# Kernel optimization log

Measured on AMD Instinct MI355X. Metric: run time of the kernel, lower is better.

## Reference

```python
import jax, jax.numpy as jnp
import numpy as np
import math

N_FRAG = 500_000
N_GENES = 5000
N_FREQ = 20
ENC_DIM = N_FREQ * 2 * 2  # 80
EMB_DIM = 5


def setup_inputs() -> dict:
    key = jax.random.key(0)
    k1, k2, k3, k4 = jax.random.split(key, 4)
    coordinates = jax.random.normal(k1, (N_FRAG, 2), dtype=jnp.float32) * 1000.0
    gene_ix = jax.random.randint(k2, (N_FRAG,), 0, N_GENES, dtype=jnp.int64 if jax.config.jax_enable_x64 else jnp.int32)
    # disjoint contiguous groups covering all fragments: 100k groups of 2, 50k of 3, 25k of 4, 10k of 5
    n2 = jnp.arange(0, 200_000, dtype=jnp.int32)
    n3 = jnp.arange(200_000, 350_000, dtype=jnp.int32)
    n4 = jnp.arange(350_000, 450_000, dtype=jnp.int32)
    n5 = jnp.arange(450_000, 500_000, dtype=jnp.int32)
    stdv = 1.0 / math.sqrt(EMB_DIM)
    weight1 = jax.random.uniform(k3, (N_GENES, ENC_DIM, EMB_DIM), dtype=jnp.float32, minval=-stdv, maxval=stdv)
    weight2 = jax.random.uniform(k4, (N_GENES, ENC_DIM, EMB_DIM), dtype=jnp.float32, minval=-stdv, maxval=stdv)
    return {"coordinates": coordinates, "gene_ix": gene_ix, "n2": n2, "n3": n3, "n4": n4, "n5": n5,
            "weight1": weight1, "weight2": weight2}


def _sine_encoding(coordinates):
    # frequencies: each of the N_FREQ frequencies repeated twice; shifts alternate (0, pi/2)
    i = jnp.arange(1, N_FREQ + 1, dtype=coordinates.dtype)
    freqs = jnp.repeat(1.0 / 1000.0 ** (2.0 * i / N_FREQ), 2)            # [2*N_FREQ]
    shifts = jnp.tile(jnp.array([0.0, jnp.pi / 2], coordinates.dtype), N_FREQ)  # [2*N_FREQ]
    # [N, 2, 1] * [2*N_FREQ] -> [N, 2, 2*N_FREQ] -> flatten -> [N, ENC_DIM]
    return jnp.sin(coordinates[..., None] * freqs + shifts).reshape(coordinates.shape[0], -1)


def _group_self_attention(emb, enc_dim_unused, groups):
    # groups: list of (group_size, flat index array); disjoint sets of fragment rows
    D = emb.shape[-1]
    for i, n_ in groups:
        x = emb[n_].reshape(-1, i, D)                                    # [G, i, D]
        scores = jnp.einsum('gid,gjd->gij', x, x) / math.sqrt(i)         # scale by sqrt(group size)
        y = jnp.einsum('gij,gjd->gid', jax.nn.softmax(scores, axis=-1), x)
        emb = emb.at[n_].set(y.reshape(-1, D))
    return emb


def reference(coordinates, gene_ix, n2, n3, n4, n5, weight1, weight2):
    enc = _sine_encoding(coordinates)                                    # [N, 80]
    # per-fragment gather of gene weight matrix, contract over encoding dim
    emb = jax.nn.sigmoid(jnp.einsum('ne,ned->nd', enc, weight1[gene_ix]))  # [N, 5]
    # NOTE: original forward computes embedding_att from weight2 but never uses it (dead code)
    emb = _group_self_attention(emb, enc, [(2, n2), (3, n3), (4, n4), (5, n5)])
    return emb
```

## Files before the change

### kernel.cpp

```cpp
#include <hip/hip_runtime.h>
#include <hip/hip_bf16.h>
#include <math.h>

#define N_FRAG 500000
#define N_GENES 5000
#define EMB_DIM 5
#define NFREQ 20
#define NR 8
#define SECCAP 64
#define GCAP (NR * SECCAP)
#define CURSTRIDE 16
#define CURN 5120
#define SCAT_BLOCKS ((N_FRAG + 255) / 256)
#define CHUNKS_PER_GENE 3
#define NTASKS (N_GENES * CHUNKS_PER_GENE)
#define EMB_BLOCKS ((NTASKS + 3) / 4)
#define ATTN_BLOCKS 723

static constexpr float FREQS[20] = {
    5.011872336272722e-01f, 2.511886431509580e-01f, 1.258925411794167e-01f,
    6.309573444801933e-02f, 3.162277660168379e-02f, 1.584893192461113e-02f,
    7.943282347242814e-03f, 3.981071705534973e-03f, 1.995262314968880e-03f,
    1.000000000000000e-03f, 5.011872336272725e-04f, 2.511886431509580e-04f,
    1.258925411794167e-04f, 6.309573444801934e-05f, 3.162277660168379e-05f,
    1.584893192461114e-05f, 7.943282347242822e-06f, 3.981071705534973e-06f,
    1.995262314968879e-06f, 1.000000000000000e-06f
};
#define INV2PI 0.15915494309189535f

__global__ void __launch_bounds__(256) scatter_xcd_kernel(
    const int* __restrict__ gene_ix,
    int* __restrict__ cursor, int* __restrict__ sortedN)
{
    int xcd;
    asm volatile("s_getreg_b32 %0, hwreg(HW_REG_XCC_ID)" : "=s"(xcd));
    const int r = xcd & (NR - 1);

    int i = blockIdx.x * blockDim.x + threadIdx.x;
    if (i >= N_FRAG) return;
    int g = gene_ix[i];
    int pos = atomicAdd(&cursor[((size_t)r * CURN + g) * CURSTRIDE], 1);
    if (pos < SECCAP)
        sortedN[(size_t)g * GCAP + r * SECCAP + pos] = i;
}

__global__ void __launch_bounds__(256) emb_wave_kernel(
    const int* __restrict__ cursor, const int* __restrict__ sortedN,
    const float* __restrict__ coords, const float* __restrict__ w1,
    float* __restrict__ out)
{
    __shared__ float wlds[4][400];
    const int wv   = threadIdx.x >> 6;
    const int lane = threadIdx.x & 63;
    const int task = blockIdx.x * 4 + wv;
    if (task >= NTASKS) return;
    const int g     = task / CHUNKS_PER_GENE;
    const int chunk = task - CHUNKS_PER_GENE * g;

    int c0 = min(cursor[((size_t)0 * CURN + g) * CURSTRIDE], SECCAP);
    int c1 = min(cursor[((size_t)1 * CURN + g) * CURSTRIDE], SECCAP);
    int c2 = min(cursor[((size_t)2 * CURN + g) * CURSTRIDE], SECCAP);
    int c3 = min(cursor[((size_t)3 * CURN + g) * CURSTRIDE], SECCAP);
    int c4 = min(cursor[((size_t)4 * CURN + g) * CURSTRIDE], SECCAP);
    int c5 = min(cursor[((size_t)5 * CURN + g) * CURSTRIDE], SECCAP);
    int c6 = min(cursor[((size_t)6 * CURN + g) * CURSTRIDE], SECCAP);
    int c7 = min(cursor[((size_t)7 * CURN + g) * CURSTRIDE], SECCAP);
    int S1 = c0, S2 = S1 + c1, S3 = S2 + c2, S4 = S3 + c3;
    int S5 = S4 + c4, S6 = S5 + c5, S7 = S6 + c6;
    int total = S7 + c7;

    if (chunk * 64 >= total) return;

    const float4* __restrict__ Wg4 =
        reinterpret_cast<const float4*>(w1 + (size_t)g * 400);
    float4* wl4 = reinterpret_cast<float4*>(&wlds[wv][0]);
    if (lane < 50) {
        float4 wa = Wg4[lane];
        float4 wb = Wg4[lane + 50];
        wl4[lane]      = wa;
        wl4[lane + 50] = wb;
    }

    const int cid = chunk * 64 + lane;
    const bool active = cid < total;

    int r = (cid >= S1) + (cid >= S2) + (cid >= S3) + (cid >= S4)
          + (cid >= S5) + (cid >= S6) + (cid >= S7);
    int Sr = 0;
    Sr = (r == 1) ? S1 : Sr;  Sr = (r == 2) ? S2 : Sr;
    Sr = (r == 3) ? S3 : Sr;  Sr = (r == 4) ? S4 : Sr;
    Sr = (r == 5) ? S5 : Sr;  Sr = (r == 6) ? S6 : Sr;
    Sr = (r == 7) ? S7 : Sr;
    int idx = cid - Sr;

    float cx = 0.f, cy = 0.f; int n = 0;
    if (active) {
        n = sortedN[(size_t)g * GCAP + r * SECCAP + idx];
        float2 c = reinterpret_cast<const float2*>(coords)[n];
        cx = c.x; cy = c.y;
    }

    const float* __restrict__ W = &wlds[wv][0];
    float a0 = 0.f, a1 = 0.f, a2 = 0.f, a3 = 0.f, a4 = 0.f;
#pragma unroll
    for (int k = 0; k < NFREQ; ++k) {
        const float gf = FREQS[k] * INV2PI;
        float rx = cx * gf; rx -= floorf(rx);
        float ry = cy * gf; ry -= floorf(ry);
        float s0 = __builtin_amdgcn_sinf(rx);
        float c0f = __builtin_amdgcn_cosf(rx);
        float s1 = __builtin_amdgcn_sinf(ry);
        float c1f = __builtin_amdgcn_cosf(ry);

        const float* p0 = W + 10 * k;
        const float* p1 = W + 200 + 10 * k;
        a0 = fmaf(s0, p0[0], fmaf(c0f, p0[5], fmaf(s1, p1[0], fmaf(c1f, p1[5], a0))));
        a1 = fmaf(s0, p0[1], fmaf(c0f, p0[6], fmaf(s1, p1[1], fmaf(c1f, p1[6], a1))));
        a2 = fmaf(s0, p0[2], fmaf(c0f, p0[7], fmaf(s1, p1[2], fmaf(c1f, p1[7], a2))));
        a3 = fmaf(s0, p0[3], fmaf(c0f, p0[8], fmaf(s1, p1[3], fmaf(c1f, p1[8], a3))));
        a4 = fmaf(s0, p0[4], fmaf(c0f, p0[9], fmaf(s1, p1[4], fmaf(c1f, p1[9], a4))));
    }

    if (active) {
        float* o = out + (size_t)n * EMB_DIM;
        o[0] = 1.f / (1.f + __expf(-a0));
        o[1] = 1.f / (1.f + __expf(-a1));
        o[2] = 1.f / (1.f + __expf(-a2));
        o[3] = 1.f / (1.f + __expf(-a3));
        o[4] = 1.f / (1.f + __expf(-a4));
    }
}

template <int S>
__device__ __forceinline__ void attn_one_inplace(float* __restrict__ p) {
    float x[S][EMB_DIM];
#pragma unroll
    for (int i = 0; i < S; ++i)
#pragma unroll
        for (int d = 0; d < EMB_DIM; ++d) x[i][d] = p[i * EMB_DIM + d];
    const float inv_scale = 1.f / sqrtf((float)S);
    float y[S][EMB_DIM];
#pragma unroll
    for (int i = 0; i < S; ++i) {
        float sc[S]; float m = -1e30f;
#pragma unroll
        for (int j = 0; j < S; ++j) {
            float s = 0.f;
#pragma unroll
            for (int d = 0; d < EMB_DIM; ++d) s = fmaf(x[i][d], x[j][d], s);
            sc[j] = s * inv_scale; m = fmaxf(m, sc[j]);
        }
        float sum = 0.f;
#pragma unroll
        for (int j = 0; j < S; ++j) { sc[j] = __expf(sc[j] - m); sum += sc[j]; }
        float r = 1.f / sum;
#pragma unroll
        for (int d = 0; d < EMB_DIM; ++d) {
            float a = 0.f;
#pragma unroll
            for (int j = 0; j < S; ++j) a = fmaf(sc[j], x[j][d], a);
            y[i][d] = a * r;
        }
    }
#pragma unroll
    for (int i = 0; i < S; ++i)
#pragma unroll
        for (int d = 0; d < EMB_DIM; ++d) p[i * EMB_DIM + d] = y[i][d];
}

__global__ void __launch_bounds__(256) attn_inplace_kernel(float* __restrict__ out) {
    int t = blockIdx.x * blockDim.x + threadIdx.x;
    if (t < 100000)      attn_one_inplace<2>(out + (size_t)(2 * t) * EMB_DIM);
    else if (t < 150000) attn_one_inplace<3>(out + (size_t)(200000 + 3 * (t - 100000)) * EMB_DIM);
    else if (t < 175000) attn_one_inplace<4>(out + (size_t)(350000 + 4 * (t - 150000)) * EMB_DIM);
    else if (t < 185000) attn_one_inplace<5>(out + (size_t)(450000 + 5 * (t - 175000)) * EMB_DIM);
}

__global__ void __launch_bounds__(256) emb_direct_kernel(
    const float* __restrict__ coords,
    const int* __restrict__ gene_ix,
    const float* __restrict__ weight1,
    float* __restrict__ out)
{
    int n = blockIdx.x * blockDim.x + threadIdx.x;
    if (n >= N_FRAG) return;
    float cx = coords[2 * n], cy = coords[2 * n + 1];
    float enc[80];
#pragma unroll
    for (int i = 0; i < NFREQ; ++i) {
        const float g = FREQS[i] * INV2PI;
        float rx = cx * g; rx -= floorf(rx);
        float ry = cy * g; ry -= floorf(ry);
        enc[2 * i]          = __builtin_amdgcn_sinf(rx);
        enc[2 * i + 1]      = __builtin_amdgcn_cosf(rx);
        enc[40 + 2 * i]     = __builtin_amdgcn_sinf(ry);
        enc[40 + 2 * i + 1] = __builtin_amdgcn_cosf(ry);
    }
    const float4* __restrict__ W4 =
        reinterpret_cast<const float4*>(weight1 + (size_t)gene_ix[n] * 400);
    float acc[EMB_DIM] = {0.f, 0.f, 0.f, 0.f, 0.f};
#pragma unroll
    for (int j = 0; j < 100; ++j) {
        float4 w = W4[j];
        const int k0 = 4 * j;
        acc[(k0 + 0) % 5] = fmaf(enc[(k0 + 0) / 5], w.x, acc[(k0 + 0) % 5]);
        acc[(k0 + 1) % 5] = fmaf(enc[(k0 + 1) / 5], w.y, acc[(k0 + 1) % 5]);
        acc[(k0 + 2) % 5] = fmaf(enc[(k0 + 2) / 5], w.z, acc[(k0 + 2) % 5]);
        acc[(k0 + 3) % 5] = fmaf(enc[(k0 + 3) / 5], w.w, acc[(k0 + 3) % 5]);
    }
    float* o = out + (size_t)n * EMB_DIM;
#pragma unroll
    for (int d = 0; d < EMB_DIM; ++d)
        o[d] = 1.f / (1.f + __expf(-acc[d]));
}

extern "C" void kernel_launch(void* const* d_in, const int* in_sizes, int n_in,
                              void* d_out, int out_size, void* d_ws, size_t ws_size,
                              hipStream_t stream) {
    const float* coords  = (const float*)d_in[0];
    const int*   gene_ix = (const int*)d_in[1];
    const float* weight1 = (const float*)d_in[6];
    float* out = (float*)d_out;

    const size_t cursor_bytes = (size_t)NR * CURN * CURSTRIDE * 4;
    const size_t off_cursor   = 0;
    const size_t off_sortedN  = 0x280000;
    const size_t need         = off_sortedN + (size_t)N_GENES * GCAP * 4;

    if (ws_size >= need) {
        int* cursor  = (int*)((char*)d_ws + off_cursor);
        int* sortedN = (int*)((char*)d_ws + off_sortedN);

        hipMemsetAsync(cursor, 0, cursor_bytes, stream);
        scatter_xcd_kernel<<<SCAT_BLOCKS, 256, 0, stream>>>(gene_ix, cursor, sortedN);
        emb_wave_kernel<<<EMB_BLOCKS, 256, 0, stream>>>(
            cursor, sortedN, coords, weight1, out);
        attn_inplace_kernel<<<ATTN_BLOCKS, 256, 0, stream>>>(out);
    } else {
        const int nb_frag = (N_FRAG + 255) / 256;
        emb_direct_kernel<<<nb_frag, 256, 0, stream>>>(coords, gene_ix, weight1, out);
        attn_inplace_kernel<<<ATTN_BLOCKS, 256, 0, stream>>>(out);
    }
}
```

Measured before the change: 61.67 us.

## Scatter coordinates into gene-sorted slots and gather embeddings in attention

The scatter kernel now copies each fragment's coordinates into its gene-sorted slot and records an inverse slot map, replacing the stored fragment index. The embedding kernel reads coordinates contiguously and writes sigmoid outputs to a slot-ordered buffer instead of scattering them into the output. A new attention kernel gathers each group's rows through the inverse map and writes coalesced results to the output. This moves the random accesses from the embedding stage into the scatter and attention stages, at the cost of extra workspace traffic and an additional indirection per fragment.

After: 64.79 us. +5.1%, slower.

```diff
diff --git a/kernel.cpp b/kernel.cpp
--- a/kernel.cpp
+++ b/kernel.cpp
@@ -29,8 +29,8 @@
 #define INV2PI 0.15915494309189535f
 
 __global__ void __launch_bounds__(256) scatter_xcd_kernel(
-    const int* __restrict__ gene_ix,
-    int* __restrict__ cursor, int* __restrict__ sortedN)
+    const int* __restrict__ gene_ix, const float* __restrict__ coords,
+    int* __restrict__ cursor, float2* __restrict__ cg2, int* __restrict__ inv)
 {
     int xcd;
     asm volatile("s_getreg_b32 %0, hwreg(HW_REG_XCC_ID)" : "=s"(xcd));
@@ -40,14 +40,16 @@
     if (i >= N_FRAG) return;
     int g = gene_ix[i];
     int pos = atomicAdd(&cursor[((size_t)r * CURN + g) * CURSTRIDE], 1);
-    if (pos < SECCAP)
-        sortedN[(size_t)g * GCAP + r * SECCAP + pos] = i;
+    if (pos < SECCAP) {
+        int slot = g * GCAP + r * SECCAP + pos;
+        cg2[slot] = reinterpret_cast<const float2*>(coords)[i];
+        inv[i] = slot;
+    }
 }
 
 __global__ void __launch_bounds__(256) emb_wave_kernel(
-    const int* __restrict__ cursor, const int* __restrict__ sortedN,
-    const float* __restrict__ coords, const float* __restrict__ w1,
-    float* __restrict__ out)
+    const int* __restrict__ cursor, const float2* __restrict__ cg2,
+    const float* __restrict__ w1, float* __restrict__ embS)
 {
     __shared__ float wlds[4][400];
     const int wv   = threadIdx.x >> 6;
@@ -92,11 +94,11 @@
     Sr = (r == 5) ? S5 : Sr;  Sr = (r == 6) ? S6 : Sr;
     Sr = (r == 7) ? S7 : Sr;
     int idx = cid - Sr;
-
-    float cx = 0.f, cy = 0.f; int n = 0;
+    int slot = g * GCAP + r * SECCAP + idx;
+
+    float cx = 0.f, cy = 0.f;
     if (active) {
-        n = sortedN[(size_t)g * GCAP + r * SECCAP + idx];
-        float2 c = reinterpret_cast<const float2*>(coords)[n];
+        float2 c = cg2[slot];
         cx = c.x; cy = c.y;
     }
 
@@ -122,13 +124,71 @@
     }
 
     if (active) {
-        float* o = out + (size_t)n * EMB_DIM;
-        o[0] = 1.f / (1.f + __expf(-a0));
-        o[1] = 1.f / (1.f + __expf(-a1));
-        o[2] = 1.f / (1.f + __expf(-a2));
-        o[3] = 1.f / (1.f + __expf(-a3));
-        o[4] = 1.f / (1.f + __expf(-a4));
-    }
+        float* e = embS + (size_t)slot * EMB_DIM;
+        e[0] = 1.f / (1.f + __expf(-a0));
+        e[1] = 1.f / (1.f + __expf(-a1));
+        e[2] = 1.f / (1.f + __expf(-a2));
+        e[3] = 1.f / (1.f + __expf(-a3));
+        e[4] = 1.f / (1.f + __expf(-a4));
+    }
+}
+
+template <int S>
+__device__ __forceinline__ void attn_one_gather(
+    const float* __restrict__ embS, const int* __restrict__ inv,
+    int r0, float* __restrict__ out)
+{
+    float x[S][EMB_DIM];
+#pragma unroll
+    for (int m = 0; m < S; ++m) {
+        int slot = inv[r0 + m];
+        const float* e = embS + (size_t)slot * EMB_DIM;
+#pragma unroll
+        for (int d = 0; d < EMB_DIM; ++d) x[m][d] = e[d];
+    }
+
+    const float inv_scale = 1.f / sqrtf((float)S);
+    float y[S][EMB_DIM];
+#pragma unroll
+    for (int i = 0; i < S; ++i) {
+        float sc[S]; float m = -1e30f;
+#pragma unroll
+        for (int j = 0; j < S; ++j) {
+            float s = 0.f;
+#pragma unroll
+            for (int d = 0; d < EMB_DIM; ++d) s = fmaf(x[i][d], x[j][d], s);
+            sc[j] = s * inv_scale; m = fmaxf(m, sc[j]);
+        }
+        float sum = 0.f;
+#pragma unroll
+        for (int j = 0; j < S; ++j) { sc[j] = __expf(sc[j] - m); sum += sc[j]; }
+        float rr = 1.f / sum;
+#pragma unroll
+        for (int d = 0; d < EMB_DIM; ++d) {
+            float a = 0.f;
+#pragma unroll
+            for (int j = 0; j < S; ++j) a = fmaf(sc[j], x[j][d], a);
+            y[i][d] = a * rr;
+        }
+    }
+
+    float* o = out + (size_t)r0 * EMB_DIM;
+#pragma unroll
+    for (int i = 0; i < S; ++i)
+#pragma unroll
+        for (int d = 0; d < EMB_DIM; ++d)
+            o[i * EMB_DIM + d] = y[i][d];
+}
+
+__global__ void __launch_bounds__(256) attn_gather_kernel(
+    const float* __restrict__ embS, const int* __restrict__ inv,
+    float* __restrict__ out)
+{
+    int t = blockIdx.x * blockDim.x + threadIdx.x;
+    if (t < 100000)      attn_one_gather<2>(embS, inv, 2 * t, out);
+    else if (t < 150000) attn_one_gather<3>(embS, inv, 200000 + 3 * (t - 100000), out);
+    else if (t < 175000) attn_one_gather<4>(embS, inv, 350000 + 4 * (t - 150000), out);
+    else if (t < 185000) attn_one_gather<5>(embS, inv, 450000 + 5 * (t - 175000), out);
 }
 
 template <int S>
@@ -223,19 +283,23 @@
     float* out = (float*)d_out;
 
     const size_t cursor_bytes = (size_t)NR * CURN * CURSTRIDE * 4;
-    const size_t off_cursor   = 0;
-    const size_t off_sortedN  = 0x280000;
-    const size_t need         = off_sortedN + (size_t)N_GENES * GCAP * 4;
+    const size_t off_cursor = 0;
+    const size_t off_cg2    = 0x280000;
+    const size_t off_inv    = 0x1608000;
+    const size_t off_embS   = 0x1800000;
+    const size_t need       = off_embS + (size_t)N_GENES * GCAP * EMB_DIM * 4;
 
     if (ws_size >= need) {
-        int* cursor  = (int*)((char*)d_ws + off_cursor);
-        int* sortedN = (int*)((char*)d_ws + off_sortedN);
+        int*    cursor = (int*)((char*)d_ws + off_cursor);
+        float2* cg2    = (float2*)((char*)d_ws + off_cg2);
+        int*    inv    = (int*)((char*)d_ws + off_inv);
+        float*  embS   = (float*)((char*)d_ws + off_embS);
 
         hipMemsetAsync(cursor, 0, cursor_bytes, stream);
-        scatter_xcd_kernel<<<SCAT_BLOCKS, 256, 0, stream>>>(gene_ix, cursor, sortedN);
-        emb_wave_kernel<<<EMB_BLOCKS, 256, 0, stream>>>(
-            cursor, sortedN, coords, weight1, out);
-        attn_inplace_kernel<<<ATTN_BLOCKS, 256, 0, stream>>>(out);
+        scatter_xcd_kernel<<<SCAT_BLOCKS, 256, 0, stream>>>(
+            gene_ix, coords, cursor, cg2, inv);
+        emb_wave_kernel<<<EMB_BLOCKS, 256, 0, stream>>>(cursor, cg2, weight1, embS);
+        attn_gather_kernel<<<ATTN_BLOCKS, 256, 0, stream>>>(embS, inv, out);
     } else {
         const int nb_frag = (N_FRAG + 255) / 256;
         emb_direct_kernel<<<nb_frag, 256, 0, stream>>>(coords, gene_ix, weight1, out);
```
